# Kernel optimization log

Measured on AMD Instinct MI355X. Metric: run time of the kernel, lower is better.

## Reference

```python
import jax, jax.numpy as jnp
import numpy as np


def setup_inputs() -> dict:
    key = jax.random.key(0)
    kx, ky = jax.random.split(key)
    x = jax.random.normal(kx, (8192, 256), dtype=jnp.float32)
    y = jax.random.normal(ky, (8192, 256), dtype=jnp.float32)
    return {"x": x, "y": y, "gamma": 1.0}


def reference(x, y, gamma):
    # RBF kernel: exp(-gamma * ||x_i - y_j||^2), computed without the
    x_sq = jnp.sum(x * x, axis=-1)            # [N]
    y_sq = jnp.sum(y * y, axis=-1)            # [M]
    cross = jnp.einsum('nd,md->nm', x, y)     # [N, M]
    sq_dist = x_sq[:, None] + y_sq[None, :] - 2.0 * cross
    sq_dist = jnp.maximum(sq_dist, 0.0)       # guard tiny negatives from fp error
    return jnp.exp(-gamma * sq_dist)
```

## Files before the change

### kernel.cpp

```cpp
#include <hip/hip_runtime.h>

#define NR 8192
#define DK 256
#define BM 128
#define BN 128
#define BK 64

typedef __bf16 bf16x8 __attribute__((ext_vector_type(8)));
typedef float f32x4 __attribute__((ext_vector_type(4)));
typedef unsigned short ushort_t;
typedef unsigned int uint_t;

__device__ __forceinline__ ushort_t f2bf(float f) {
  uint_t u = __float_as_uint(f);
  u += 0x7fffu + ((u >> 16) & 1u);
  return (ushort_t)(u >> 16);
}

__global__ __launch_bounds__(256) void prep_kernel(
    const float* __restrict__ x, const float* __restrict__ y,
    ushort_t* __restrict__ xb, ushort_t* __restrict__ yb,
    float* __restrict__ xsq, float* __restrict__ ysq) {
  int row = blockIdx.x * 4 + (threadIdx.x >> 6);
  int lane = threadIdx.x & 63;
  const float* src; ushort_t* dst; float* sq; int r;
  if (row < NR) { src = x; dst = xb; sq = xsq; r = row; }
  else          { src = y; dst = yb; sq = ysq; r = row - NR; }
  float4 v = ((const float4*)(src + (size_t)r * DK))[lane];
  float s = v.x * v.x + v.y * v.y + v.z * v.z + v.w * v.w;
  ushort4 o;
  o.x = f2bf(v.x); o.y = f2bf(v.y); o.z = f2bf(v.z); o.w = f2bf(v.w);
  ((ushort4*)(dst + (size_t)r * DK))[lane] = o;
#pragma unroll
  for (int off = 32; off; off >>= 1) s += __shfl_xor(s, off, 64);
  if (lane == 0) sq[r] = s;
}

__global__ __launch_bounds__(256) void rbf_gemm(
    const ushort_t* __restrict__ xb, const ushort_t* __restrict__ yb,
    const float* __restrict__ xsq, const float* __restrict__ ysq,
    const float* __restrict__ gptr, float* __restrict__ out) {
  __shared__ ushort_t lds[2 * BM * BK];
  ushort_t* ldsA = lds;
  ushort_t* ldsB = lds + BM * BK;

  const int t = threadIdx.x;
  const int wid = t >> 6, lane = t & 63;
  const int wm = wid >> 1, wn = wid & 1;
  const int tm = blockIdx.x, tn = blockIdx.y;

  f32x4 acc[4][4];
#pragma unroll
  for (int i = 0; i < 4; ++i)
#pragma unroll
    for (int j = 0; j < 4; ++j)
      acc[i][j] = (f32x4){0.f, 0.f, 0.f, 0.f};

  const int c_row = t >> 3;
  const int c_col = (((t & 7) ^ ((t >> 3) & 7)) * 8);

  for (int kt = 0; kt < DK / BK; ++kt) {
    const int k0 = kt * BK;
#pragma unroll
    for (int s = 0; s < 4; ++s) {
      const ushort_t* gA = xb + (size_t)(tm * BM + s * 32 + c_row) * DK + k0 + c_col;
      const ushort_t* gB = yb + (size_t)(tn * BN + s * 32 + c_row) * DK + k0 + c_col;
      char* lA = (char*)ldsA + s * 4096 + wid * 1024;
      char* lB = (char*)ldsB + s * 4096 + wid * 1024;
      __builtin_amdgcn_global_load_lds(
          (const __attribute__((address_space(1))) void*)gA,
          (__attribute__((address_space(3))) void*)lA, 16, 0, 0);
      __builtin_amdgcn_global_load_lds(
          (const __attribute__((address_space(1))) void*)gB,
          (__attribute__((address_space(3))) void*)lB, 16, 0, 0);
    }
    __syncthreads();

    {
      const int fr = lane & 15, fk = lane >> 4;
      bf16x8 af[4][2], bfr[4][2];
#pragma unroll
      for (int i = 0; i < 4; ++i) {
#pragma unroll
        for (int kk = 0; kk < 2; ++kk) {
          const int rowA = wm * 64 + i * 16 + fr;
          const int slotA = (kk * 4 + fk) ^ (rowA & 7);
          af[i][kk] = *(const bf16x8*)((const char*)ldsA + rowA * 128 + slotA * 16);
          const int rowB = wn * 64 + i * 16 + fr;
          const int slotB = (kk * 4 + fk) ^ (rowB & 7);
          bfr[i][kk] = *(const bf16x8*)((const char*)ldsB + rowB * 128 + slotB * 16);
        }
      }
#pragma unroll
      for (int i = 0; i < 4; ++i)
#pragma unroll
        for (int j = 0; j < 4; ++j)
#pragma unroll
          for (int kk = 0; kk < 2; ++kk)
            acc[i][j] = __builtin_amdgcn_mfma_f32_16x16x32_bf16(
                af[i][kk], bfr[j][kk], acc[i][j], 0, 0, 0);
    }
    __syncthreads();
  }

  const float gamma = *gptr;
  const int fr = lane & 15, fq = lane >> 4;
  const int rowbase = tm * BM + wm * 64;
  const int colbase = tn * BN + wn * 64;
#pragma unroll
  for (int i = 0; i < 4; ++i) {
    float xs[4];
#pragma unroll
    for (int r = 0; r < 4; ++r)
      xs[r] = xsq[rowbase + i * 16 + fq * 4 + r];
#pragma unroll
    for (int j = 0; j < 4; ++j) {
      const int gcol = colbase + j * 16 + fr;
      const float yv = ysq[gcol];
#pragma unroll
      for (int r = 0; r < 4; ++r) {
        const int grow = rowbase + i * 16 + fq * 4 + r;
        float d = xs[r] + yv - 2.0f * acc[i][j][r];
        d = fmaxf(d, 0.0f);
        out[(size_t)grow * NR + gcol] = __expf(-gamma * d);
      }
    }
  }
}

extern "C" void kernel_launch(void* const* d_in, const int* in_sizes, int n_in,
                              void* d_out, int out_size, void* d_ws, size_t ws_size,
                              hipStream_t stream) {
  const float* x = (const float*)d_in[0];
  const float* y = (const float*)d_in[1];
  const float* gamma = (const float*)d_in[2];
  float* out = (float*)d_out;
  char* ws = (char*)d_ws;
  ushort_t* xb = (ushort_t*)ws;
  ushort_t* yb = (ushort_t*)(ws + (size_t)NR * DK * 2);
  float* xsq = (float*)(ws + (size_t)NR * DK * 4);
  float* ysq = (float*)(ws + (size_t)NR * DK * 4 + (size_t)NR * 4);

  prep_kernel<<<dim3((2 * NR) / 4), dim3(256), 0, stream>>>(x, y, xb, yb, xsq, ysq);
  rbf_gemm<<<dim3(NR / BM, NR / BN), dim3(256), 0, stream>>>(xb, yb, xsq, ysq, gamma, out);
}
```

Baseline: 294.1 us.

## Swizzle block order, raise occupancy hint, stream A fragments per row tile

Remaps the flat block index so consecutive workgroups are spread across tile rows and columns, which changes L2 and XCD locality for operand reuse. Adds a min-blocks-per-CU launch bound of 4 to cap register use. Loads A fragments one row-tile at a time inside the MFMA loop instead of all up front, cutting live registers. This may add LDS latency stalls between MFMAs.

Result: slower. 372.1 us (+26.5%).

```diff
diff --git a/kernel.cpp b/kernel.cpp
--- a/kernel.cpp
+++ b/kernel.cpp
@@ -36,7 +36,7 @@
   if (lane == 0) sq[r] = s;
 }
 
-__global__ __launch_bounds__(256) void rbf_gemm(
+__global__ __launch_bounds__(256, 4) void rbf_gemm(
     const ushort_t* __restrict__ xb, const ushort_t* __restrict__ yb,
     const float* __restrict__ xsq, const float* __restrict__ ysq,
     const float* __restrict__ gptr, float* __restrict__ out) {
@@ -47,7 +47,11 @@
   const int t = threadIdx.x;
   const int wid = t >> 6, lane = t & 63;
   const int wm = wid >> 1, wn = wid & 1;
-  const int tm = blockIdx.x, tn = blockIdx.y;
+
+  const int flat = blockIdx.y * gridDim.x + blockIdx.x;
+  const int swz = (flat & 7) * 512 + (flat >> 3);
+  const int tm = swz & 63;
+  const int tn = swz >> 6;
 
   f32x4 acc[4][4];
 #pragma unroll
@@ -78,27 +82,29 @@
 
     {
       const int fr = lane & 15, fk = lane >> 4;
-      bf16x8 af[4][2], bfr[4][2];
+      bf16x8 bfr[4][2];
 #pragma unroll
-      for (int i = 0; i < 4; ++i) {
+      for (int j = 0; j < 4; ++j) {
 #pragma unroll
         for (int kk = 0; kk < 2; ++kk) {
-          const int rowA = wm * 64 + i * 16 + fr;
-          const int slotA = (kk * 4 + fk) ^ (rowA & 7);
-          af[i][kk] = *(const bf16x8*)((const char*)ldsA + rowA * 128 + slotA * 16);
-          const int rowB = wn * 64 + i * 16 + fr;
+          const int rowB = wn * 64 + j * 16 + fr;
           const int slotB = (kk * 4 + fk) ^ (rowB & 7);
-          bfr[i][kk] = *(const bf16x8*)((const char*)ldsB + rowB * 128 + slotB * 16);
+          bfr[j][kk] = *(const bf16x8*)((const char*)ldsB + rowB * 128 + slotB * 16);
         }
       }
 #pragma unroll
-      for (int i = 0; i < 4; ++i)
+      for (int i = 0; i < 4; ++i) {
+        const int rowA = wm * 64 + i * 16 + fr;
+        const int slotA0 = (0 * 4 + fk) ^ (rowA & 7);
+        const int slotA1 = (1 * 4 + fk) ^ (rowA & 7);
+        bf16x8 a0 = *(const bf16x8*)((const char*)ldsA + rowA * 128 + slotA0 * 16);
+        bf16x8 a1 = *(const bf16x8*)((const char*)ldsA + rowA * 128 + slotA1 * 16);
 #pragma unroll
-        for (int j = 0; j < 4; ++j)
-#pragma unroll
-          for (int kk = 0; kk < 2; ++kk)
-            acc[i][j] = __builtin_amdgcn_mfma_f32_16x16x32_bf16(
-                af[i][kk], bfr[j][kk], acc[i][j], 0, 0, 0);
+        for (int j = 0; j < 4; ++j) {
+          acc[i][j] = __builtin_amdgcn_mfma_f32_16x16x32_bf16(a0, bfr[j][0], acc[i][j], 0, 0, 0);
+          acc[i][j] = __builtin_amdgcn_mfma_f32_16x16x32_bf16(a1, bfr[j][1], acc[i][j], 0, 0, 0);
+        }
+      }
     }
     __syncthreads();
   }
```
